# Kernel optimization log

Hardware: AMD Instinct MI355X
Metric: run time of the kernel (lower is better)

The kernel has to match this reference:

```python
import jax, jax.numpy as jnp
import numpy as np

H = 768  # sparse grid height
W = 768  # sparse grid width
N = 200000  # active sites
CIN = 256
CB = 64


def setup_inputs() -> dict:
    key = jax.random.key(0)
    ks = jax.random.split(key, 11)
    rng = np.random.default_rng(0)
    # unique active-site linear coordinates on the HxW grid
    coords = jnp.asarray(np.sort(rng.choice(H * W, N, replace=False)).astype(np.int64))
    feats = jax.random.normal(ks[0], (N, CIN), jnp.float32)
    w1 = jax.random.normal(ks[1], (CIN, CB), jnp.float32) / np.float32(np.sqrt(CIN))
    w2 = jax.random.normal(ks[2], (9, CB, CB), jnp.float32) / np.float32(np.sqrt(9 * CB))
    w3 = jax.random.normal(ks[3], (CB, CIN), jnp.float32) / np.float32(np.sqrt(CB))
    s1 = jax.random.uniform(ks[4], (CB,), jnp.float32, 0.5, 1.5)
    b1 = jax.random.normal(ks[5], (CB,), jnp.float32) * 0.1
    s2 = jax.random.uniform(ks[6], (CB,), jnp.float32, 0.5, 1.5)
    b2 = jax.random.normal(ks[7], (CB,), jnp.float32) * 0.1
    s3 = jax.random.uniform(ks[8], (CIN,), jnp.float32, 0.5, 1.5)
    b3 = jax.random.normal(ks[9], (CIN,), jnp.float32) * 0.1
    return dict(feats=feats, coords=coords, w1=w1, w2=w2, w3=w3,
                s1=s1, b1=b1, s2=s2, b2=b2, s3=s3, b3=b3)


def sparse_conv3x3(feats, coords, w2):
    # active-site sparse 3x3 conv: gather valid neighbors, matmul per tap, accumulate
    idx_map = jnp.full((H * W,), -1, jnp.int32).at[coords].set(
        jnp.arange(N, dtype=jnp.int32))
    y, x = coords // W, coords % W
    out = jnp.zeros((N, w2.shape[2]), feats.dtype)
    k = 0
    for dy in (-1, 0, 1):
        for dx in (-1, 0, 1):
            ny, nx = y + dy, x + dx
            inb = (ny >= 0) & (ny < H) & (nx >= 0) & (nx < W)
            lin = jnp.clip(ny, 0, H - 1) * W + jnp.clip(nx, 0, W - 1)
            r = idx_map[lin]
            ok = inb & (r >= 0)
            g = jnp.where(ok[:, None], feats[jnp.maximum(r, 0)], 0.0)
            out = out + g @ w2[k]
            k += 1
    return out


def reference(feats, coords, w1, w2, w3, s1, b1, s2, b2, s3, b3):
    identity = feats
    out = jax.nn.relu((feats @ w1) * s1 + b1)            # conv1 1x1 + bn1 + relu
    out = jax.nn.relu(sparse_conv3x3(out, coords, w2) * s2 + b2)  # conv2 3x3 + bn2 + relu
    out = (out @ w3) * s3 + b3                            # conv3 1x1 + bn3
    return jax.nn.relu(out + identity)                    # residual + relu
```

## Files before the change

### kernel.cpp

```cpp
#include <hip/hip_runtime.h>
#include <hip/hip_bf16.h>
#include <stdint.h>

#define HH 768
#define WW 768
#define NN 200000
#define CI 256
#define CB 64

typedef __attribute__((ext_vector_type(8))) __bf16 bf16x8;
typedef __attribute__((ext_vector_type(4))) float f32x4;
typedef __attribute__((ext_vector_type(4))) unsigned short u16x4;

__device__ inline unsigned short f2bf(float f) {
    union { float f; unsigned int i; } v; v.f = f;
    unsigned int r = v.i + 0x7FFF + ((v.i >> 16) & 1);
    return (unsigned short)(r >> 16);
}
__device__ inline f32x4 mfma16(bf16x8 a, bf16x8 b, f32x4 c) {
    return __builtin_amdgcn_mfma_f32_16x16x32_bf16(a, b, c, 0, 0, 0);
}
__device__ inline bf16x8 ldfrag(const unsigned short* p) {
    return *(const bf16x8*)p;
}
__device__ inline bf16x8 ldfrag_f32(const float* p) {
    float4 f0 = *(const float4*)(p);
    float4 f1 = *(const float4*)(p + 4);
    bf16x8 a;
    a[0] = (__bf16)f0.x; a[1] = (__bf16)f0.y; a[2] = (__bf16)f0.z; a[3] = (__bf16)f0.w;
    a[4] = (__bf16)f1.x; a[5] = (__bf16)f1.y; a[6] = (__bf16)f1.z; a[7] = (__bf16)f1.w;
    return a;
}


__global__ void k_scatter(const int* __restrict__ coords, int* __restrict__ idx_map) {
    int i = blockIdx.x * 256 + threadIdx.x;
    if (i < NN) idx_map[coords[i]] = i;
}

__global__ void k_prepw(const float* __restrict__ w1,
                        const float* __restrict__ w2,
                        const float* __restrict__ w3,
                        unsigned short* __restrict__ w1t,
                        unsigned short* __restrict__ w2t,
                        unsigned short* __restrict__ w3t) {
    int tid = blockIdx.x * 256 + threadIdx.x;
    int stride = gridDim.x * 256;
    for (int i = tid; i < CI * CB; i += stride) {
        int k = i / CB, n = i % CB;
        w1t[n * CI + k] = f2bf(w1[i]);
    }
    for (int i = tid; i < 9 * CB * CB; i += stride) {
        int t = i / (CB * CB), rem = i % (CB * CB);
        int k = rem / CB, n = rem % CB;
        w2t[t * CB * CB + n * CB + k] = f2bf(w2[i]);
    }
    for (int i = tid; i < CB * CI; i += stride) {
        int k = i / CI, n = i % CI;
        w3t[n * CB + k] = f2bf(w3[i]);
    }
}


__global__ __launch_bounds__(256, 4) void k_gemm1(const float* __restrict__ feats,
                                                  const unsigned short* __restrict__ w1t,
                                                  const float* __restrict__ s1,
                                                  const float* __restrict__ b1,
                                                  unsigned short* __restrict__ out1) {
    const int wave = threadIdx.x >> 6;
    const int lane = threadIdx.x & 63;
    const int m = lane & 15;
    const int quad = lane >> 4;
    const int row0 = blockIdx.x * 128 + wave * 32;
    if (row0 >= NN) return;

    f32x4 acc[2][4];
#pragma unroll
    for (int rt = 0; rt < 2; ++rt)
#pragma unroll
        for (int ct = 0; ct < 4; ++ct) acc[rt][ct] = (f32x4){0.f, 0.f, 0.f, 0.f};

#pragma unroll
    for (int ks = 0; ks < 8; ++ks) {
        bf16x8 f[2];
#pragma unroll
        for (int rt = 0; rt < 2; ++rt)
            f[rt] = ldfrag_f32(feats + (size_t)(row0 + rt * 16 + m) * CI + quad * 8 + ks * 32);
#pragma unroll
        for (int ct = 0; ct < 4; ++ct) {
            bf16x8 b = ldfrag(w1t + (ct * 16 + m) * CI + quad * 8 + ks * 32);
#pragma unroll
            for (int rt = 0; rt < 2; ++rt)
                acc[rt][ct] = mfma16(b, f[rt], acc[rt][ct]);
        }
    }

#pragma unroll
    for (int rt = 0; rt < 2; ++rt)
#pragma unroll
        for (int ct = 0; ct < 4; ++ct) {
            int row = row0 + rt * 16 + m;
            int c0 = ct * 16 + quad * 4;
            float4 sc = *(const float4*)(s1 + c0);
            float4 bi = *(const float4*)(b1 + c0);
            float v0 = acc[rt][ct][0] * sc.x + bi.x;
            float v1 = acc[rt][ct][1] * sc.y + bi.y;
            float v2 = acc[rt][ct][2] * sc.z + bi.z;
            float v3 = acc[rt][ct][3] * sc.w + bi.w;
            u16x4 o;
            o.x = f2bf(v0 > 0.f ? v0 : 0.f);
            o.y = f2bf(v1 > 0.f ? v1 : 0.f);
            o.z = f2bf(v2 > 0.f ? v2 : 0.f);
            o.w = f2bf(v3 > 0.f ? v3 : 0.f);
            *(u16x4*)(out1 + (size_t)row * CB + c0) = o;
        }
}


__global__ __launch_bounds__(256, 2) void k_conv3(const unsigned short* __restrict__ out1,
                                                  const unsigned short* __restrict__ w2t,
                                                  const unsigned short* __restrict__ w3t,
                                                  const int* __restrict__ coords,
                                                  const int* __restrict__ idx_map,
                                                  const float* __restrict__ s2,
                                                  const float* __restrict__ b2,
                                                  const float* __restrict__ s3,
                                                  const float* __restrict__ b3,
                                                  const unsigned short* __restrict__ zrow,
                                                  const float* __restrict__ feats,
                                                  float* __restrict__ out) {
    __shared__ int s_nbr[128 * 9];
    __shared__ unsigned short s_x[4][32][68];

    const int tid = threadIdx.x;
    const int wave = tid >> 6;
    const int lane = tid & 63;
    const int m = lane & 15;
    const int quad = lane >> 4;
    const int row0 = blockIdx.x * 128 + wave * 32;
    const bool live = (row0 < NN);

    float4 fr[2][2][4];
    if (live) {
#pragma unroll
        for (int rt = 0; rt < 2; ++rt)
#pragma unroll
            for (int ct = 0; ct < 4; ++ct)
                fr[0][rt][ct] = *(const float4*)(feats + (size_t)(row0 + rt * 16 + m) * CI
                                                 + ct * 16 + quad * 4);
    }

    if (tid < 128) {
        int grow = blockIdx.x * 128 + tid;
        if (grow < NN) {
            int c = coords[grow];
            int y = c / WW, x = c - y * WW;
#pragma unroll
            for (int t = 0; t < 9; ++t) {
                int dy = t / 3 - 1, dx = t % 3 - 1;
                int ny = y + dy, nx = x + dx;
                int r = -1;
                if (ny >= 0 && ny < HH && nx >= 0 && nx < WW) r = idx_map[ny * WW + nx];
                s_nbr[tid * 9 + t] = r;
            }
        } else {
#pragma unroll
            for (int t = 0; t < 9; ++t) s_nbr[tid * 9 + t] = -1;
        }
    }
    __syncthreads();
    if (!live) return;

    f32x4 acc[2][4];
#pragma unroll
    for (int rt = 0; rt < 2; ++rt)
#pragma unroll
        for (int ct = 0; ct < 4; ++ct) acc[rt][ct] = (f32x4){0.f, 0.f, 0.f, 0.f};

#pragma unroll
    for (int t = 0; t < 9; ++t) {
        bf16x8 a[2][2];
#pragma unroll
        for (int rt = 0; rt < 2; ++rt) {
            int r = s_nbr[(wave * 32 + rt * 16 + m) * 9 + t];
            const unsigned short* base = (r >= 0) ? (out1 + (size_t)r * CB) : zrow;
            a[rt][0] = ldfrag(base + quad * 8);
            a[rt][1] = ldfrag(base + quad * 8 + 32);
        }
#pragma unroll
        for (int ks = 0; ks < 2; ++ks)
#pragma unroll
            for (int ct = 0; ct < 4; ++ct) {
                bf16x8 b = ldfrag(w2t + t * CB * CB + (ct * 16 + m) * CB + quad * 8 + ks * 32);
#pragma unroll
                for (int rt = 0; rt < 2; ++rt)
                    acc[rt][ct] = mfma16(b, a[rt][ks], acc[rt][ct]);
            }
    }

#pragma unroll
    for (int rt = 0; rt < 2; ++rt)
#pragma unroll
        for (int ct = 0; ct < 4; ++ct) {
            int c0 = ct * 16 + quad * 4;
            float4 sc = *(const float4*)(s2 + c0);
            float4 bi = *(const float4*)(b2 + c0);
            float v0 = acc[rt][ct][0] * sc.x + bi.x;
            float v1 = acc[rt][ct][1] * sc.y + bi.y;
            float v2 = acc[rt][ct][2] * sc.z + bi.z;
            float v3 = acc[rt][ct][3] * sc.w + bi.w;
            u16x4 o;
            o.x = f2bf(v0 > 0.f ? v0 : 0.f);
            o.y = f2bf(v1 > 0.f ? v1 : 0.f);
            o.z = f2bf(v2 > 0.f ? v2 : 0.f);
            o.w = f2bf(v3 > 0.f ? v3 : 0.f);
            *(u16x4*)&s_x[wave][rt * 16 + m][c0] = o;
        }

    bf16x8 a3[2][2];
#pragma unroll
    for (int rt = 0; rt < 2; ++rt)
#pragma unroll
        for (int ks = 0; ks < 2; ++ks)
            a3[rt][ks] = ldfrag(&s_x[wave][rt * 16 + m][ks * 32 + quad * 8]);

#pragma unroll
    for (int cc = 0; cc < 4; ++cc) {
        if (cc < 3) {
#pragma unroll
            for (int rt = 0; rt < 2; ++rt)
#pragma unroll
                for (int ct = 0; ct < 4; ++ct)
                    fr[(cc + 1) & 1][rt][ct] =
                        *(const float4*)(feats + (size_t)(row0 + rt * 16 + m) * CI
                                         + (cc + 1) * 64 + ct * 16 + quad * 4);
        }

        const int cbase = cc * 64;
        f32x4 acc3[2][4];
#pragma unroll
        for (int rt = 0; rt < 2; ++rt)
#pragma unroll
            for (int ct = 0; ct < 4; ++ct) acc3[rt][ct] = (f32x4){0.f, 0.f, 0.f, 0.f};

#pragma unroll
        for (int ks = 0; ks < 2; ++ks)
#pragma unroll
            for (int ct = 0; ct < 4; ++ct) {
                bf16x8 b = ldfrag(w3t + (cbase + ct * 16 + m) * CB + quad * 8 + ks * 32);
#pragma unroll
                for (int rt = 0; rt < 2; ++rt)
                    acc3[rt][ct] = mfma16(b, a3[rt][ks], acc3[rt][ct]);
            }

#pragma unroll
        for (int rt = 0; rt < 2; ++rt)
#pragma unroll
            for (int ct = 0; ct < 4; ++ct) {
                int row = row0 + rt * 16 + m;
                int c0 = cbase + ct * 16 + quad * 4;
                float4 sc = *(const float4*)(s3 + c0);
                float4 bi = *(const float4*)(b3 + c0);
                float4 f = fr[cc & 1][rt][ct];
                float4 v;
                v.x = acc3[rt][ct][0] * sc.x + bi.x + f.x;
                v.y = acc3[rt][ct][1] * sc.y + bi.y + f.y;
                v.z = acc3[rt][ct][2] * sc.z + bi.z + f.z;
                v.w = acc3[rt][ct][3] * sc.w + bi.w + f.w;
                v.x = v.x > 0.f ? v.x : 0.f;
                v.y = v.y > 0.f ? v.y : 0.f;
                v.z = v.z > 0.f ? v.z : 0.f;
                v.w = v.w > 0.f ? v.w : 0.f;
                *(float4*)(out + (size_t)row * CI + c0) = v;
            }
    }
}


extern "C" void kernel_launch(void* const* d_in, const int* in_sizes, int n_in,
                              void* d_out, int out_size, void* d_ws, size_t ws_size,
                              hipStream_t stream) {
    const float* feats = (const float*)d_in[0];
    const int* coords = (const int*)d_in[1];
    const float* w1 = (const float*)d_in[2];
    const float* w2 = (const float*)d_in[3];
    const float* w3 = (const float*)d_in[4];
    const float* s1 = (const float*)d_in[5];
    const float* b1 = (const float*)d_in[6];
    const float* s2 = (const float*)d_in[7];
    const float* b2 = (const float*)d_in[8];
    const float* s3 = (const float*)d_in[9];
    const float* b3 = (const float*)d_in[10];
    float* out = (float*)d_out;

    char* ws = (char*)d_ws;
    int* idx_map        = (int*)(ws + 0);
    unsigned short* w1t = (unsigned short*)(ws + 2359296);
    unsigned short* w2t = (unsigned short*)(ws + 2392064);
    unsigned short* w3t = (unsigned short*)(ws + 2465792);
    unsigned short* out1= (unsigned short*)(ws + 2498560);
    unsigned short* zrow= (unsigned short*)(ws + 53698560);

    hipMemsetAsync(idx_map, 0xFF, (size_t)HH * WW * 4, stream);
    hipMemsetAsync(zrow, 0x00, 128, stream);
    k_scatter<<<(NN + 255) / 256, 256, 0, stream>>>(coords, idx_map);
    k_prepw<<<64, 256, 0, stream>>>(w1, w2, w3, w1t, w2t, w3t);
    k_gemm1<<<(NN + 127) / 128, 256, 0, stream>>>(feats, w1t, s1, b1, out1);
    k_conv3<<<(NN + 127) / 128, 256, 0, stream>>>(out1, w2t, w3t, coords, idx_map,
                                                  s2, b2, s3, b3, zrow, feats, out);
}
```

Measured before the change: 535.7 us.

## Double-buffer gathers and weights, widen per-wave tiles to 64 rows

```diff
diff --git a/kernel.cpp b/kernel.cpp
--- a/kernel.cpp
+++ b/kernel.cpp
@@ -12,6 +12,8 @@
 typedef __attribute__((ext_vector_type(4))) float f32x4;
 typedef __attribute__((ext_vector_type(4))) unsigned short u16x4;
 
+#define SGB __builtin_amdgcn_sched_group_barrier
+
 __device__ inline unsigned short f2bf(float f) {
     union { float f; unsigned int i; } v; v.f = f;
     unsigned int r = v.i + 0x7FFF + ((v.i >> 16) & 1);
@@ -23,9 +25,7 @@
 __device__ inline bf16x8 ldfrag(const unsigned short* p) {
     return *(const bf16x8*)p;
 }
-__device__ inline bf16x8 ldfrag_f32(const float* p) {
-    float4 f0 = *(const float4*)(p);
-    float4 f1 = *(const float4*)(p + 4);
+__device__ inline bf16x8 cvt8(float4 f0, float4 f1) {
     bf16x8 a;
     a[0] = (__bf16)f0.x; a[1] = (__bf16)f0.y; a[2] = (__bf16)f0.z; a[3] = (__bf16)f0.w;
     a[4] = (__bf16)f1.x; a[5] = (__bf16)f1.y; a[6] = (__bf16)f1.z; a[7] = (__bf16)f1.w;
@@ -62,7 +62,7 @@
 }
 
 
-__global__ __launch_bounds__(256, 4) void k_gemm1(const float* __restrict__ feats,
+__global__ __launch_bounds__(256, 2) void k_gemm1(const float* __restrict__ feats,
                                                   const unsigned short* __restrict__ w1t,
                                                   const float* __restrict__ s1,
                                                   const float* __restrict__ b1,
@@ -71,32 +71,60 @@
     const int lane = threadIdx.x & 63;
     const int m = lane & 15;
     const int quad = lane >> 4;
-    const int row0 = blockIdx.x * 128 + wave * 32;
+    const int row0 = blockIdx.x * 256 + wave * 64;
     if (row0 >= NN) return;
 
-    f32x4 acc[2][4];
-#pragma unroll
-    for (int rt = 0; rt < 2; ++rt)
+    const float* arow[4];
+#pragma unroll
+    for (int rt = 0; rt < 4; ++rt)
+        arow[rt] = feats + (size_t)(row0 + rt * 16 + m) * CI + quad * 8;
+
+    f32x4 acc[4][4];
+#pragma unroll
+    for (int rt = 0; rt < 4; ++rt)
 #pragma unroll
         for (int ct = 0; ct < 4; ++ct) acc[rt][ct] = (f32x4){0.f, 0.f, 0.f, 0.f};
 
+    float4 araw[2][4][2];
+    bf16x8 bfr[2][4];
+#pragma unroll
+    for (int rt = 0; rt < 4; ++rt) {
+        araw[0][rt][0] = *(const float4*)(arow[rt]);
+        araw[0][rt][1] = *(const float4*)(arow[rt] + 4);
+    }
+#pragma unroll
+    for (int ct = 0; ct < 4; ++ct)
+        bfr[0][ct] = ldfrag(w1t + (ct * 16 + m) * CI + quad * 8);
+
 #pragma unroll
     for (int ks = 0; ks < 8; ++ks) {
-        bf16x8 f[2];
-#pragma unroll
-        for (int rt = 0; rt < 2; ++rt)
-            f[rt] = ldfrag_f32(feats + (size_t)(row0 + rt * 16 + m) * CI + quad * 8 + ks * 32);
-#pragma unroll
-        for (int ct = 0; ct < 4; ++ct) {
-            bf16x8 b = ldfrag(w1t + (ct * 16 + m) * CI + quad * 8 + ks * 32);
-#pragma unroll
-            for (int rt = 0; rt < 2; ++rt)
-                acc[rt][ct] = mfma16(b, f[rt], acc[rt][ct]);
-        }
-    }
-
-#pragma unroll
-    for (int rt = 0; rt < 2; ++rt)
+        const int cur = ks & 1, nxt = cur ^ 1;
+        bf16x8 af[4];
+#pragma unroll
+        for (int rt = 0; rt < 4; ++rt)
+            af[rt] = cvt8(araw[cur][rt][0], araw[cur][rt][1]);
+        if (ks < 7) {
+#pragma unroll
+            for (int rt = 0; rt < 4; ++rt) {
+                araw[nxt][rt][0] = *(const float4*)(arow[rt] + (ks + 1) * 32);
+                araw[nxt][rt][1] = *(const float4*)(arow[rt] + (ks + 1) * 32 + 4);
+            }
+#pragma unroll
+            for (int ct = 0; ct < 4; ++ct)
+                bfr[nxt][ct] = ldfrag(w1t + (ct * 16 + m) * CI + quad * 8 + (ks + 1) * 32);
+        }
+#pragma unroll
+        for (int ct = 0; ct < 4; ++ct)
+#pragma unroll
+            for (int rt = 0; rt < 4; ++rt)
+                acc[rt][ct] = mfma16(bfr[cur][ct], af[rt], acc[rt][ct]);
+        SGB(0x2, 16, 0);
+        SGB(0x20, 12, 0);
+        SGB(0x8, 16, 0);
+    }
+
+#pragma unroll
+    for (int rt = 0; rt < 4; ++rt)
 #pragma unroll
         for (int ct = 0; ct < 4; ++ct) {
             int row = row0 + rt * 16 + m;
@@ -129,29 +157,19 @@
                                                   const unsigned short* __restrict__ zrow,
                                                   const float* __restrict__ feats,
                                                   float* __restrict__ out) {
-    __shared__ int s_nbr[128 * 9];
-    __shared__ unsigned short s_x[4][32][68];
+    __shared__ int s_nbr[256 * 9];
+    __shared__ unsigned short s_x[256][68];
 
     const int tid = threadIdx.x;
     const int wave = tid >> 6;
     const int lane = tid & 63;
     const int m = lane & 15;
     const int quad = lane >> 4;
-    const int row0 = blockIdx.x * 128 + wave * 32;
+    const int row0 = blockIdx.x * 256 + wave * 64;
     const bool live = (row0 < NN);
 
-    float4 fr[2][2][4];
-    if (live) {
-#pragma unroll
-        for (int rt = 0; rt < 2; ++rt)
-#pragma unroll
-            for (int ct = 0; ct < 4; ++ct)
-                fr[0][rt][ct] = *(const float4*)(feats + (size_t)(row0 + rt * 16 + m) * CI
-                                                 + ct * 16 + quad * 4);
-    }
-
-    if (tid < 128) {
-        int grow = blockIdx.x * 128 + tid;
+    {
+        int grow = blockIdx.x * 256 + tid;
         if (grow < NN) {
             int c = coords[grow];
             int y = c / WW, x = c - y * WW;
@@ -171,35 +189,60 @@
     __syncthreads();
     if (!live) return;
 
-    f32x4 acc[2][4];
-#pragma unroll
-    for (int rt = 0; rt < 2; ++rt)
+    f32x4 acc[4][4];
+#pragma unroll
+    for (int rt = 0; rt < 4; ++rt)
 #pragma unroll
         for (int ct = 0; ct < 4; ++ct) acc[rt][ct] = (f32x4){0.f, 0.f, 0.f, 0.f};
 
+    bf16x8 ga[2][4][2];
+    bf16x8 wb[2][2][4];
+
+#pragma unroll
+    for (int rt = 0; rt < 4; ++rt) {
+        int r = s_nbr[(wave * 64 + rt * 16 + m) * 9 + 0];
+        const unsigned short* base = (r >= 0) ? (out1 + (size_t)r * CB) : zrow;
+        ga[0][rt][0] = ldfrag(base + quad * 8);
+        ga[0][rt][1] = ldfrag(base + quad * 8 + 32);
+    }
+#pragma unroll
+    for (int ks = 0; ks < 2; ++ks)
+#pragma unroll
+        for (int ct = 0; ct < 4; ++ct)
+            wb[0][ks][ct] = ldfrag(w2t + (ct * 16 + m) * CB + quad * 8 + ks * 32);
+
 #pragma unroll
     for (int t = 0; t < 9; ++t) {
-        bf16x8 a[2][2];
-#pragma unroll
-        for (int rt = 0; rt < 2; ++rt) {
-            int r = s_nbr[(wave * 32 + rt * 16 + m) * 9 + t];
-            const unsigned short* base = (r >= 0) ? (out1 + (size_t)r * CB) : zrow;
-            a[rt][0] = ldfrag(base + quad * 8);
-            a[rt][1] = ldfrag(base + quad * 8 + 32);
+        const int cur = t & 1, nxt = cur ^ 1;
+        if (t < 8) {
+#pragma unroll
+            for (int rt = 0; rt < 4; ++rt) {
+                int r = s_nbr[(wave * 64 + rt * 16 + m) * 9 + t + 1];
+                const unsigned short* base = (r >= 0) ? (out1 + (size_t)r * CB) : zrow;
+                ga[nxt][rt][0] = ldfrag(base + quad * 8);
+                ga[nxt][rt][1] = ldfrag(base + quad * 8 + 32);
+            }
+#pragma unroll
+            for (int ks = 0; ks < 2; ++ks)
+#pragma unroll
+                for (int ct = 0; ct < 4; ++ct)
+                    wb[nxt][ks][ct] = ldfrag(w2t + (t + 1) * CB * CB
+                                             + (ct * 16 + m) * CB + quad * 8 + ks * 32);
         }
 #pragma unroll
         for (int ks = 0; ks < 2; ++ks)
 #pragma unroll
-            for (int ct = 0; ct < 4; ++ct) {
-                bf16x8 b = ldfrag(w2t + t * CB * CB + (ct * 16 + m) * CB + quad * 8 + ks * 32);
-#pragma unroll
-                for (int rt = 0; rt < 2; ++rt)
-                    acc[rt][ct] = mfma16(b, a[rt][ks], acc[rt][ct]);
-            }
-    }
-
-#pragma unroll
-    for (int rt = 0; rt < 2; ++rt)
+            for (int ct = 0; ct < 4; ++ct)
+#pragma unroll
+                for (int rt = 0; rt < 4; ++rt)
+                    acc[rt][ct] = mfma16(wb[cur][ks][ct], ga[cur][rt][ks], acc[rt][ct]);
+        SGB(0x100, 4, 0);
+        SGB(0x20, 16, 0);
+        SGB(0x8, 32, 0);
+    }
+
+#pragma unroll
+    for (int rt = 0; rt < 4; ++rt)
 #pragma unroll
         for (int ct = 0; ct < 4; ++ct) {
             int c0 = ct * 16 + quad * 4;
@@ -214,54 +257,58 @@
             o.y = f2bf(v1 > 0.f ? v1 : 0.f);
             o.z = f2bf(v2 > 0.f ? v2 : 0.f);
             o.w = f2bf(v3 > 0.f ? v3 : 0.f);
-            *(u16x4*)&s_x[wave][rt * 16 + m][c0] = o;
-        }
-
-    bf16x8 a3[2][2];
-#pragma unroll
-    for (int rt = 0; rt < 2; ++rt)
+            *(u16x4*)&s_x[wave * 64 + rt * 16 + m][c0] = o;
+        }
+
+    bf16x8 a3[4][2];
+#pragma unroll
+    for (int rt = 0; rt < 4; ++rt)
 #pragma unroll
         for (int ks = 0; ks < 2; ++ks)
-            a3[rt][ks] = ldfrag(&s_x[wave][rt * 16 + m][ks * 32 + quad * 8]);
+            a3[rt][ks] = ldfrag(&s_x[wave * 64 + rt * 16 + m][ks * 32 + quad * 8]);
 
 #pragma unroll
     for (int cc = 0; cc < 4; ++cc) {
-        if (cc < 3) {
-#pragma unroll
-            for (int rt = 0; rt < 2; ++rt)
-#pragma unroll
-                for (int ct = 0; ct < 4; ++ct)
-                    fr[(cc + 1) & 1][rt][ct] =
-                        *(const float4*)(feats + (size_t)(row0 + rt * 16 + m) * CI
-                                         + (cc + 1) * 64 + ct * 16 + quad * 4);
-        }
-
         const int cbase = cc * 64;
-        f32x4 acc3[2][4];
-#pragma unroll
-        for (int rt = 0; rt < 2; ++rt)
+
+        float4 res[4][4];
+#pragma unroll
+        for (int rt = 0; rt < 4; ++rt)
+#pragma unroll
+            for (int ct = 0; ct < 4; ++ct)
+                res[rt][ct] = *(const float4*)(feats + (size_t)(row0 + rt * 16 + m) * CI
+                                               + cbase + ct * 16 + quad * 4);
+
+        bf16x8 w3f[2][4];
+#pragma unroll
+        for (int ks = 0; ks < 2; ++ks)
+#pragma unroll
+            for (int ct = 0; ct < 4; ++ct)
+                w3f[ks][ct] = ldfrag(w3t + (cbase + ct * 16 + m) * CB + quad * 8 + ks * 32);
+
+        f32x4 acc3[4][4];
+#pragma unroll
+        for (int rt = 0; rt < 4; ++rt)
 #pragma unroll
             for (int ct = 0; ct < 4; ++ct) acc3[rt][ct] = (f32x4){0.f, 0.f, 0.f, 0.f};
 
 #pragma unroll
         for (int ks = 0; ks < 2; ++ks)
 #pragma unroll
-            for (int ct = 0; ct < 4; ++ct) {
-                bf16x8 b = ldfrag(w3t + (cbase + ct * 16 + m) * CB + quad * 8 + ks * 32);
-#pragma unroll
-                for (int rt = 0; rt < 2; ++rt)
-                    acc3[rt][ct] = mfma16(b, a3[rt][ks], acc3[rt][ct]);
-            }
-
-#pragma unroll
-        for (int rt = 0; rt < 2; ++rt)
+            for (int ct = 0; ct < 4; ++ct)
+#pragma unroll
+                for (int rt = 0; rt < 4; ++rt)
+                    acc3[rt][ct] = mfma16(w3f[ks][ct], a3[rt][ks], acc3[rt][ct]);
+
+#pragma unroll
+        for (int rt = 0; rt < 4; ++rt)
 #pragma unroll
             for (int ct = 0; ct < 4; ++ct) {
                 int row = row0 + rt * 16 + m;
                 int c0 = cbase + ct * 16 + quad * 4;
                 float4 sc = *(const float4*)(s3 + c0);
                 float4 bi = *(const float4*)(b3 + c0);
-                float4 f = fr[cc & 1][rt][ct];
+                float4 f = res[rt][ct];
                 float4 v;
                 v.x = acc3[rt][ct][0] * sc.x + bi.x + f.x;
                 v.y = acc3[rt][ct][1] * sc.y + bi.y + f.y;
@@ -273,6 +320,9 @@
                 v.w = v.w > 0.f ? v.w : 0.f;
                 *(float4*)(out + (size_t)row * CI + c0) = v;
             }
+        SGB(0x20, 24, 0);
+        SGB(0x8, 32, 0);
+        SGB(0x40, 16, 0);
     }
 }
 
@@ -305,7 +355,7 @@
     hipMemsetAsync(zrow, 0x00, 128, stream);
     k_scatter<<<(NN + 255) / 256, 256, 0, stream>>>(coords, idx_map);
     k_prepw<<<64, 256, 0, stream>>>(w1, w2, w3, w1t, w2t, w3t);
-    k_gemm1<<<(NN + 127) / 128, 256, 0, stream>>>(feats, w1t, s1, b1, out1);
-    k_conv3<<<(NN + 127) / 128, 256, 0, stream>>>(out1, w2t, w3t, coords, idx_map,
+    k_gemm1<<<(NN + 255) / 256, 256, 0, stream>>>(feats, w1t, s1, b1, out1);
+    k_conv3<<<(NN + 255) / 256, 256, 0, stream>>>(out1, w2t, w3t, coords, idx_map,
                                                   s2, b2, s3, b3, zrow, feats, out);
 }
```

New measurement: 539.4 us. No clear change (+0.7%).

## Stage feats via async global-to-LDS DMA and enlarge conv tile to 64 rows per wave

Applied to the files above, without the earlier changes.

```diff
diff --git a/kernel.cpp b/kernel.cpp
--- a/kernel.cpp
+++ b/kernel.cpp
@@ -23,14 +23,19 @@
 __device__ inline bf16x8 ldfrag(const unsigned short* p) {
     return *(const bf16x8*)p;
 }
-__device__ inline bf16x8 ldfrag_f32(const float* p) {
-    float4 f0 = *(const float4*)(p);
-    float4 f1 = *(const float4*)(p + 4);
+__device__ inline bf16x8 cvt8(float4 f0, float4 f1) {
     bf16x8 a;
     a[0] = (__bf16)f0.x; a[1] = (__bf16)f0.y; a[2] = (__bf16)f0.z; a[3] = (__bf16)f0.w;
     a[4] = (__bf16)f1.x; a[5] = (__bf16)f1.y; a[6] = (__bf16)f1.z; a[7] = (__bf16)f1.w;
     return a;
 }
+__device__ inline void dma16(const float* g, float* lds_base_uniform) {
+    __builtin_amdgcn_global_load_lds(
+        (const __attribute__((address_space(1))) unsigned int*)g,
+        (__attribute__((address_space(3))) unsigned int*)lds_base_uniform, 16, 0, 0);
+}
+#define FENCE() __builtin_amdgcn_sched_barrier(0)
+#define LGKM0() do { asm volatile("s_waitcnt lgkmcnt(0)" ::: "memory"); FENCE(); } while (0)
 
 
 __global__ void k_scatter(const int* __restrict__ coords, int* __restrict__ idx_map) {
@@ -67,6 +72,8 @@
                                                   const float* __restrict__ s1,
                                                   const float* __restrict__ b1,
                                                   unsigned short* __restrict__ out1) {
+    __shared__ float sA[4][2][32][32];
+
     const int wave = threadIdx.x >> 6;
     const int lane = threadIdx.x & 63;
     const int m = lane & 15;
@@ -74,25 +81,56 @@
     const int row0 = blockIdx.x * 128 + wave * 32;
     if (row0 >= NN) return;
 
+    const int srow = lane >> 3;
+    const int sc4 = (lane & 7) ^ srow;
+    const float* fbase = feats + (size_t)(row0 + srow) * CI + sc4 * 4;
+
+    auto stageA = [&](int ks, int b) {
+#pragma unroll
+        for (int j = 0; j < 4; ++j)
+            dma16(fbase + (size_t)(j * 8) * CI + ks * 32, &sA[wave][b][j * 8][0]);
+    };
+
     f32x4 acc[2][4];
 #pragma unroll
     for (int rt = 0; rt < 2; ++rt)
 #pragma unroll
         for (int ct = 0; ct < 4; ++ct) acc[rt][ct] = (f32x4){0.f, 0.f, 0.f, 0.f};
 
+    stageA(0, 0);
+    stageA(1, 1);
+
 #pragma unroll
     for (int ks = 0; ks < 8; ++ks) {
-        bf16x8 f[2];
-#pragma unroll
-        for (int rt = 0; rt < 2; ++rt)
-            f[rt] = ldfrag_f32(feats + (size_t)(row0 + rt * 16 + m) * CI + quad * 8 + ks * 32);
-#pragma unroll
-        for (int ct = 0; ct < 4; ++ct) {
-            bf16x8 b = ldfrag(w1t + (ct * 16 + m) * CI + quad * 8 + ks * 32);
+        const int b = ks & 1;
+        if (ks == 0 || ks == 7) {
+            asm volatile("s_waitcnt vmcnt(4)" ::: "memory");
+        } else {
+            asm volatile("s_waitcnt vmcnt(8)" ::: "memory");
+        }
+        FENCE();
+
+        bf16x8 bfr[4];
+#pragma unroll
+        for (int ct = 0; ct < 4; ++ct)
+            bfr[ct] = ldfrag(w1t + (ct * 16 + m) * CI + quad * 8 + ks * 32);
+
+        bf16x8 af[2];
+#pragma unroll
+        for (int rt = 0; rt < 2; ++rt) {
+            const float* rp = &sA[wave][b][rt * 16 + m][0];
+            float4 f0 = *(const float4*)(rp + (((2 * quad + 0) ^ (m & 7)) * 4));
+            float4 f1 = *(const float4*)(rp + (((2 * quad + 1) ^ (m & 7)) * 4));
+            af[rt] = cvt8(f0, f1);
+        }
+        LGKM0();
+        if (ks < 6) stageA(ks + 2, b);
+
+#pragma unroll
+        for (int ct = 0; ct < 4; ++ct)
 #pragma unroll
             for (int rt = 0; rt < 2; ++rt)
-                acc[rt][ct] = mfma16(b, f[rt], acc[rt][ct]);
-        }
+                acc[rt][ct] = mfma16(bfr[ct], af[rt], acc[rt][ct]);
     }
 
 #pragma unroll
@@ -129,29 +167,32 @@
                                                   const unsigned short* __restrict__ zrow,
                                                   const float* __restrict__ feats,
                                                   float* __restrict__ out) {
-    __shared__ int s_nbr[128 * 9];
-    __shared__ unsigned short s_x[4][32][68];
+    __shared__ int s_nbr[256 * 9];
+    __shared__ unsigned short s_x[4][16][68];
+    __shared__ float s_res[2][4][64][16];
 
     const int tid = threadIdx.x;
     const int wave = tid >> 6;
     const int lane = tid & 63;
     const int m = lane & 15;
     const int quad = lane >> 4;
-    const int row0 = blockIdx.x * 128 + wave * 32;
+    const int row0 = blockIdx.x * 256 + wave * 64;
     const bool live = (row0 < NN);
 
-    float4 fr[2][2][4];
-    if (live) {
-#pragma unroll
-        for (int rt = 0; rt < 2; ++rt)
-#pragma unroll
-            for (int ct = 0; ct < 4; ++ct)
-                fr[0][rt][ct] = *(const float4*)(feats + (size_t)(row0 + rt * 16 + m) * CI
-                                                 + ct * 16 + quad * 4);
-    }
-
-    if (tid < 128) {
-        int grow = blockIdx.x * 128 + tid;
+    const int rrow = lane >> 2;
+    const int rc4 = (lane & 3) ^ (rrow & 3);
+    const float* rbase = feats + (size_t)(row0 + rrow) * CI + rc4 * 4;
+
+    auto stage_res = [&](int cc, int b) {
+#pragma unroll
+        for (int j = 0; j < 4; ++j)
+            dma16(rbase + (size_t)(j * 16) * CI + cc * 16, &s_res[b][wave][j * 16][0]);
+    };
+
+    if (live) { stage_res(0, 0); stage_res(1, 1); }
+
+    {
+        int grow = blockIdx.x * 256 + tid;
         if (grow < NN) {
             int c = coords[grow];
             int y = c / WW, x = c - y * WW;
@@ -171,35 +212,47 @@
     __syncthreads();
     if (!live) return;
 
-    f32x4 acc[2][4];
-#pragma unroll
-    for (int rt = 0; rt < 2; ++rt)
+    f32x4 acc[4][4];
+#pragma unroll
+    for (int rt = 0; rt < 4; ++rt)
 #pragma unroll
         for (int ct = 0; ct < 4; ++ct) acc[rt][ct] = (f32x4){0.f, 0.f, 0.f, 0.f};
 
+    bf16x8 ga[2][4][2];
+#pragma unroll
+    for (int rt = 0; rt < 4; ++rt) {
+        int r = s_nbr[(wave * 64 + rt * 16 + m) * 9 + 0];
+        const unsigned short* base = (r >= 0) ? (out1 + (size_t)r * CB) : zrow;
+        ga[0][rt][0] = ldfrag(base + quad * 8);
+        ga[0][rt][1] = ldfrag(base + quad * 8 + 32);
+    }
+
 #pragma unroll
     for (int t = 0; t < 9; ++t) {
-        bf16x8 a[2][2];
-#pragma unroll
-        for (int rt = 0; rt < 2; ++rt) {
-            int r = s_nbr[(wave * 32 + rt * 16 + m) * 9 + t];
-            const unsigned short* base = (r >= 0) ? (out1 + (size_t)r * CB) : zrow;
-            a[rt][0] = ldfrag(base + quad * 8);
-            a[rt][1] = ldfrag(base + quad * 8 + 32);
+        const int cur = t & 1, nxt = cur ^ 1;
+        if (t < 8) {
+#pragma unroll
+            for (int rt = 0; rt < 4; ++rt) {
+                int r = s_nbr[(wave * 64 + rt * 16 + m) * 9 + t + 1];
+                const unsigned short* base = (r >= 0) ? (out1 + (size_t)r * CB) : zrow;
+                ga[nxt][rt][0] = ldfrag(base + quad * 8);
+                ga[nxt][rt][1] = ldfrag(base + quad * 8 + 32);
+            }
         }
 #pragma unroll
         for (int ks = 0; ks < 2; ++ks)
 #pragma unroll
             for (int ct = 0; ct < 4; ++ct) {
-                bf16x8 b = ldfrag(w2t + t * CB * CB + (ct * 16 + m) * CB + quad * 8 + ks * 32);
-#pragma unroll
-                for (int rt = 0; rt < 2; ++rt)
-                    acc[rt][ct] = mfma16(b, a[rt][ks], acc[rt][ct]);
+                bf16x8 wb = ldfrag(w2t + t * CB * CB + (ct * 16 + m) * CB + quad * 8 + ks * 32);
+#pragma unroll
+                for (int rt = 0; rt < 4; ++rt)
+                    acc[rt][ct] = mfma16(wb, ga[cur][rt][ks], acc[rt][ct]);
             }
     }
 
-#pragma unroll
-    for (int rt = 0; rt < 2; ++rt)
+    bf16x8 a3[4][2];
+#pragma unroll
+    for (int rt = 0; rt < 4; ++rt) {
 #pragma unroll
         for (int ct = 0; ct < 4; ++ct) {
             int c0 = ct * 16 + quad * 4;
@@ -214,65 +267,55 @@
             o.y = f2bf(v1 > 0.f ? v1 : 0.f);
             o.z = f2bf(v2 > 0.f ? v2 : 0.f);
             o.w = f2bf(v3 > 0.f ? v3 : 0.f);
-            *(u16x4*)&s_x[wave][rt * 16 + m][c0] = o;
-        }
-
-    bf16x8 a3[2][2];
-#pragma unroll
-    for (int rt = 0; rt < 2; ++rt)
-#pragma unroll
-        for (int ks = 0; ks < 2; ++ks)
-            a3[rt][ks] = ldfrag(&s_x[wave][rt * 16 + m][ks * 32 + quad * 8]);
-
-#pragma unroll
-    for (int cc = 0; cc < 4; ++cc) {
-        if (cc < 3) {
-#pragma unroll
-            for (int rt = 0; rt < 2; ++rt)
-#pragma unroll
-                for (int ct = 0; ct < 4; ++ct)
-                    fr[(cc + 1) & 1][rt][ct] =
-                        *(const float4*)(feats + (size_t)(row0 + rt * 16 + m) * CI
-                                         + (cc + 1) * 64 + ct * 16 + quad * 4);
-        }
-
-        const int cbase = cc * 64;
-        f32x4 acc3[2][4];
-#pragma unroll
-        for (int rt = 0; rt < 2; ++rt)
-#pragma unroll
-            for (int ct = 0; ct < 4; ++ct) acc3[rt][ct] = (f32x4){0.f, 0.f, 0.f, 0.f};
-
-#pragma unroll
-        for (int ks = 0; ks < 2; ++ks)
-#pragma unroll
-            for (int ct = 0; ct < 4; ++ct) {
-                bf16x8 b = ldfrag(w3t + (cbase + ct * 16 + m) * CB + quad * 8 + ks * 32);
-#pragma unroll
-                for (int rt = 0; rt < 2; ++rt)
-                    acc3[rt][ct] = mfma16(b, a3[rt][ks], acc3[rt][ct]);
-            }
-
-#pragma unroll
-        for (int rt = 0; rt < 2; ++rt)
-#pragma unroll
-            for (int ct = 0; ct < 4; ++ct) {
-                int row = row0 + rt * 16 + m;
-                int c0 = cbase + ct * 16 + quad * 4;
-                float4 sc = *(const float4*)(s3 + c0);
-                float4 bi = *(const float4*)(b3 + c0);
-                float4 f = fr[cc & 1][rt][ct];
-                float4 v;
-                v.x = acc3[rt][ct][0] * sc.x + bi.x + f.x;
-                v.y = acc3[rt][ct][1] * sc.y + bi.y + f.y;
-                v.z = acc3[rt][ct][2] * sc.z + bi.z + f.z;
-                v.w = acc3[rt][ct][3] * sc.w + bi.w + f.w;
-                v.x = v.x > 0.f ? v.x : 0.f;
-                v.y = v.y > 0.f ? v.y : 0.f;
-                v.z = v.z > 0.f ? v.z : 0.f;
-                v.w = v.w > 0.f ? v.w : 0.f;
-                *(float4*)(out + (size_t)row * CI + c0) = v;
-            }
+            *(u16x4*)&s_x[wave][m][c0] = o;
+        }
+        a3[rt][0] = ldfrag(&s_x[wave][m][quad * 8]);
+        a3[rt][1] = ldfrag(&s_x[wave][m][32 + quad * 8]);
+    }
+
+#pragma unroll
+    for (int cc = 0; cc < 16; ++cc) {
+        const int b = cc & 1;
+        bf16x8 w3f0 = ldfrag(w3t + (cc * 16 + m) * CB + quad * 8);
+        bf16x8 w3f1 = ldfrag(w3t + (cc * 16 + m) * CB + quad * 8 + 32);
+
+        f32x4 acc3[4];
+#pragma unroll
+        for (int rt = 0; rt < 4; ++rt) acc3[rt] = (f32x4){0.f, 0.f, 0.f, 0.f};
+#pragma unroll
+        for (int rt = 0; rt < 4; ++rt) acc3[rt] = mfma16(w3f0, a3[rt][0], acc3[rt]);
+#pragma unroll
+        for (int rt = 0; rt < 4; ++rt) acc3[rt] = mfma16(w3f1, a3[rt][1], acc3[rt]);
+
+        if (cc == 0) {
+            asm volatile("s_waitcnt vmcnt(0)" ::: "memory");
+        } else {
+            asm volatile("s_waitcnt vmcnt(8)" ::: "memory");
+        }
+        FENCE();
+
+        const int c0 = cc * 16 + quad * 4;
+        float4 sc = *(const float4*)(s3 + c0);
+        float4 bi = *(const float4*)(b3 + c0);
+#pragma unroll
+        for (int rt = 0; rt < 4; ++rt) {
+            int row = rt * 16 + m;
+            float4 f = *(const float4*)&s_res[b][wave][row][(quad ^ (m & 3)) * 4];
+            float4 v;
+            v.x = acc3[rt][0] * sc.x + bi.x + f.x;
+            v.y = acc3[rt][1] * sc.y + bi.y + f.y;
+            v.z = acc3[rt][2] * sc.z + bi.z + f.z;
+            v.w = acc3[rt][3] * sc.w + bi.w + f.w;
+            v.x = v.x > 0.f ? v.x : 0.f;
+            v.y = v.y > 0.f ? v.y : 0.f;
+            v.z = v.z > 0.f ? v.z : 0.f;
+            v.w = v.w > 0.f ? v.w : 0.f;
+            *(float4*)(out + (size_t)(row0 + row) * CI + c0) = v;
+        }
+        if (cc < 14) {
+            LGKM0();
+            stage_res(cc + 2, b);
+        }
     }
 }
 
@@ -306,6 +349,6 @@
     k_scatter<<<(NN + 255) / 256, 256, 0, stream>>>(coords, idx_map);
     k_prepw<<<64, 256, 0, stream>>>(w1, w2, w3, w1t, w2t, w3t);
     k_gemm1<<<(NN + 127) / 128, 256, 0, stream>>>(feats, w1t, s1, b1, out1);
-    k_conv3<<<(NN + 127) / 128, 256, 0, stream>>>(out1, w2t, w3t, coords, idx_map,
+    k_conv3<<<(NN + 255) / 256, 256, 0, stream>>>(out1, w2t, w3t, coords, idx_map,
                                                   s2, b2, s3, b3, zrow, feats, out);
 }
```

New measurement: 533.1 us. Within noise of the previous version (-0.5%).
